# Optimization experiments

Measured on AMD Instinct MI355X. Metric: run time of the kernel, lower is better.

## Reference

```python
import jax, jax.numpy as jnp
import numpy as np

B, S, D, H, FF = 2, 2048, 1024, 16, 4096
HD = D // H          # head dim = 64
ROT = HD // 2        # rotary dim = dim/(num_heads*2) = 32 (partial rotation)
EPS = 1e-5


def setup_inputs() -> dict:
    key = jax.random.key(0)
    ks = jax.random.split(key, 16)
    std = 0.02
    return {
        "x": jax.random.normal(ks[0], (B, S, D), jnp.float32),
        "mask": jnp.ones((B, 1, 1, S), jnp.int32),
        "wq": jax.random.normal(ks[1], (D, D), jnp.float32) * std,
        "bq": jnp.zeros((D,), jnp.float32),
        "wk": jax.random.normal(ks[2], (D, D), jnp.float32) * std,
        "bk": jnp.zeros((D,), jnp.float32),
        "wv": jax.random.normal(ks[3], (D, D), jnp.float32) * std,
        "bv": jnp.zeros((D,), jnp.float32),
        "wo": jax.random.normal(ks[4], (D, D), jnp.float32) * std,
        "bo": jnp.zeros((D,), jnp.float32),
        "ln1_w": jnp.ones((D,), jnp.float32),
        "ln1_b": jnp.zeros((D,), jnp.float32),
        "ln2_w": jnp.ones((D,), jnp.float32),
        "ln2_b": jnp.zeros((D,), jnp.float32),
        "w1": jax.random.normal(ks[5], (D, FF), jnp.float32) * std,
        "b1": jnp.zeros((FF,), jnp.float32),
        "w2": jax.random.normal(ks[6], (FF, D), jnp.float32) * std,
        "b2": jnp.zeros((D,), jnp.float32),
    }


def _layernorm(x, w, b):
    mu = jnp.mean(x, axis=-1, keepdims=True)
    var = jnp.mean(jnp.square(x - mu), axis=-1, keepdims=True)
    return (x - mu) * jax.lax.rsqrt(var + EPS) * w + b


def _rope(t):
    # t: [B, H, S, HD]; rotate first ROT features, interleaved (GPT-J) pairing
    inv_freq = 1.0 / (10000.0 ** (jnp.arange(0, ROT, 2, dtype=jnp.float32) / ROT))
    ang = jnp.arange(S, dtype=jnp.float32)[:, None] * inv_freq      # [S, ROT//2]
    ang = jnp.repeat(ang, 2, axis=-1)                               # [S, ROT]
    cos, sin = jnp.cos(ang), jnp.sin(ang)
    t_rot, t_pass = t[..., :ROT], t[..., ROT:]
    pr = t_rot.reshape(*t_rot.shape[:-1], ROT // 2, 2)
    rot = jnp.stack([-pr[..., 1], pr[..., 0]], axis=-1).reshape(t_rot.shape)
    return jnp.concatenate([t_rot * cos + rot * sin, t_pass], axis=-1)


def reference(x, mask, wq, bq, wk, bk, wv, bv, wo, bo,
              ln1_w, ln1_b, ln2_w, ln2_b, w1, b1, w2, b2):
    res = x
    h = _layernorm(x, ln1_w, ln1_b)
    q = (h @ wq + bq).reshape(B, S, H, HD).transpose(0, 2, 1, 3)
    k = (h @ wk + bk).reshape(B, S, H, HD).transpose(0, 2, 1, 3)
    v = (h @ wv + bv).reshape(B, S, H, HD).transpose(0, 2, 1, 3)
    q, k = _rope(q), _rope(k)
    score = jnp.einsum('bhqd,bhkd->bhqk', q, k) * (1.0 / np.sqrt(HD))
    score = jnp.where(mask == 0, jnp.float32(-1e9), score)
    attn = jax.nn.softmax(score, axis=-1)
    out = jnp.einsum('bhqk,bhkd->bhqd', attn, v)
    out = out.transpose(0, 2, 1, 3).reshape(B, S, D) @ wo + bo
    x = res + out
    res = x
    h = _layernorm(x, ln2_w, ln2_b)
    h = jax.nn.gelu(h @ w1 + b1, approximate=False) @ w2 + b2
    return res + h
```

## Files before the change

### kernel.cpp

```cpp
#include <hip/hip_runtime.h>
#include <cstdint>
#include <cstddef>


typedef __bf16 bf16;
typedef __bf16 bf16x2 __attribute__((ext_vector_type(2)));
typedef __bf16 bf16x4v __attribute__((ext_vector_type(4)));
typedef __bf16 bf16x8 __attribute__((ext_vector_type(8)));
typedef float  f32x4  __attribute__((ext_vector_type(4)));

#define NB 2
#define NS 2048
#define ND 1024
#define NH 16
#define NHD 64
#define NFF 4096
#define NM (NB*NS)
#define QKSCALE 0.18033688011112042f

typedef uint32_t __attribute__((address_space(1))) gu32_t;
typedef uint32_t __attribute__((address_space(3))) lu32_t;
__device__ __forceinline__ void async_copy16(void* lds, const void* g) {
  __builtin_amdgcn_global_load_lds((gu32_t*)g, (lu32_t*)lds, 16, 0, 0);
}

__device__ __forceinline__ float gelu_f(float x) {
  return 0.5f * x * (1.0f + erff(x * 0.70710678118654752f));
}

__global__ __launch_bounds__(256) void prep_kernel(
    const float* __restrict__ wq, const float* __restrict__ wk,
    const float* __restrict__ wv, const float* __restrict__ wo,
    const float* __restrict__ w1, const float* __restrict__ w2,
    bf16* __restrict__ wqt, bf16* __restrict__ wkt, bf16* __restrict__ wvt,
    bf16* __restrict__ wot, bf16* __restrict__ w1t, bf16* __restrict__ w2t,
    const float* __restrict__ bq, const float* __restrict__ bk,
    const float* __restrict__ bv, float* __restrict__ bcat,
    const int* __restrict__ mask, float* __restrict__ m01f,
    bf16* __restrict__ m01b, float2* __restrict__ rtab,
    const float* __restrict__ x, const float* __restrict__ ln1w,
    const float* __restrict__ ln1b, bf16* __restrict__ h1) {
  int flat = blockIdx.x;
  int t = threadIdx.x;
  if (flat < 12288) {
    __shared__ float tile[32][33];
    const float* W; bf16* Wt; long bx, by; int K, N;
    if (flat < 4096) {
      int which = flat >> 10, r = flat & 1023;
      const float* Ws[4] = {wq, wk, wv, wo};
      bf16* Wts[4] = {wqt, wkt, wvt, wot};
      W = Ws[which]; Wt = Wts[which]; bx = r & 31; by = r >> 5; K = ND; N = ND;
    } else if (flat < 8192) {
      int r = flat - 4096;
      W = w1; Wt = w1t; bx = r & 127; by = r >> 7; K = ND; N = NFF;
    } else {
      int r = flat - 8192;
      W = w2; Wt = w2t; bx = r & 31; by = r >> 5; K = NFF; N = ND;
    }
    int tx = t & 31, ty = t >> 5;
#pragma unroll
    for (int r = 0; r < 4; ++r)
      tile[ty + r*8][tx] = W[(by*32 + ty + r*8) * (long)N + bx*32 + tx];
    __syncthreads();
#pragma unroll
    for (int r = 0; r < 4; ++r)
      Wt[(bx*32 + ty + r*8) * (long)K + by*32 + tx] = (bf16)tile[tx][ty + r*8];
  } else if (flat < 12444) {
    int blk = flat - 12288;
    if (blk < 12) {
      int i = blk * 256 + t;
      bcat[i] = (i < ND) ? bq[i] : ((i < 2*ND) ? bk[i - ND] : bv[i - 2*ND]);
    } else if (blk < 28) {
      int i = (blk - 12) * 256 + t;
      float v = mask[i] ? 1.0f : 0.0f;
      m01f[i] = v;
      m01b[i] = (bf16)v;
    } else {
      int idx = (blk - 28) * 256 + t;
      int s = idx >> 4, i = idx & 15;
      float ang = (float)s * exp2f(-(float)i * (13.287712379549449f / 16.0f));
      float sn, cs;
      sincosf(ang, &sn, &cs);
      rtab[idx] = make_float2(cs, sn);
    }
  } else {
    long row = flat - 12444;
    float4 v = ((const float4*)(x + row*ND))[t];
    float s  = v.x + v.y + v.z + v.w;
    float sq = v.x*v.x + v.y*v.y + v.z*v.z + v.w*v.w;
#pragma unroll
    for (int m = 1; m <= 32; m <<= 1) { s += __shfl_xor(s, m); sq += __shfl_xor(sq, m); }
    __shared__ float ss[4], ssq[4];
    if ((t & 63) == 0) { ss[t>>6] = s; ssq[t>>6] = sq; }
    __syncthreads();
    s  = ss[0] + ss[1] + ss[2] + ss[3];
    sq = ssq[0] + ssq[1] + ssq[2] + ssq[3];
    float mu = s * (1.0f/ND);
    float rs = rsqrtf(sq * (1.0f/ND) - mu*mu + 1e-5f);
    float4 wv4 = ((const float4*)ln1w)[t];
    float4 bv4 = ((const float4*)ln1b)[t];
    bf16x4v o;
    o[0] = (bf16)((v.x-mu)*rs*wv4.x + bv4.x);
    o[1] = (bf16)((v.y-mu)*rs*wv4.y + bv4.y);
    o[2] = (bf16)((v.z-mu)*rs*wv4.z + bv4.z);
    o[3] = (bf16)((v.w-mu)*rs*wv4.w + bv4.w);
    *(bf16x4v*)(h1 + row*ND + t*4) = o;
  }
}

__global__ __launch_bounds__(256) void vtrans_kernel(
    const bf16* __restrict__ v, bf16* __restrict__ vt) {
  __shared__ bf16 t[64][66];
  int st = blockIdx.x, bh = blockIdx.y;
  int b = bh >> 4, h = bh & 15;
  int c = threadIdx.x & 63, rg = threadIdx.x >> 6;
  const bf16* src = v + ((long)b*NS + st*64)*ND + h*64;
#pragma unroll
  for (int i = 0; i < 16; ++i) {
    int r = rg*16 + i;
    t[r][c] = src[(long)r*ND + c];
  }
  __syncthreads();
  bf16* dst = vt + (long)bh*64*NS + st*64;
#pragma unroll
  for (int i = 0; i < 16; ++i) {
    int d = rg*16 + i;
    dst[(long)d*NS + c] = t[c][d];
  }
}

__global__ __launch_bounds__(256) void ln_kernel(
    const float* __restrict__ x, const float* __restrict__ w,
    const float* __restrict__ b, bf16* __restrict__ out) {
  long row = blockIdx.x;
  int t = threadIdx.x;
  float4 v = ((const float4*)(x + row*ND))[t];
  float s  = v.x + v.y + v.z + v.w;
  float sq = v.x*v.x + v.y*v.y + v.z*v.z + v.w*v.w;
#pragma unroll
  for (int m = 1; m <= 32; m <<= 1) { s += __shfl_xor(s, m); sq += __shfl_xor(sq, m); }
  __shared__ float ss[4], ssq[4];
  if ((t & 63) == 0) { ss[t>>6] = s; ssq[t>>6] = sq; }
  __syncthreads();
  s  = ss[0] + ss[1] + ss[2] + ss[3];
  sq = ssq[0] + ssq[1] + ssq[2] + ssq[3];
  float mu = s * (1.0f/ND);
  float rs = rsqrtf(sq * (1.0f/ND) - mu*mu + 1e-5f);
  float4 wv = ((const float4*)w)[t];
  float4 bv = ((const float4*)b)[t];
  bf16x4v o;
  o[0] = (bf16)((v.x-mu)*rs*wv.x + bv.x);
  o[1] = (bf16)((v.y-mu)*rs*wv.y + bv.y);
  o[2] = (bf16)((v.z-mu)*rs*wv.z + bv.z);
  o[3] = (bf16)((v.w-mu)*rs*wv.w + bv.w);
  *(bf16x4v*)(out + row*ND + t*4) = o;
}

template<int EPI>
__global__ __launch_bounds__(512, 2) void gemm256_kernel(
    const bf16* __restrict__ A, const bf16* __restrict__ Bt,
    const float* __restrict__ bias, void* __restrict__ Cout,
    const float2* __restrict__ rtab, const float* __restrict__ m01f,
    int M, int N, int K) {
  __shared__ __align__(16) bf16 Alds[2][256*32];
  __shared__ __align__(16) bf16 Blds[2][256*32];
  const int tid = threadIdx.x, lane = tid & 63, w = tid >> 6;
  const int fr = lane & 15, kg = lane >> 4;
  const int wr = w >> 2, wc = w & 3;
  const int swb = (kg ^ ((fr >> 1) & 3)) << 4;

  const int gx = gridDim.x;
  int lin = blockIdx.y * gx + blockIdx.x;
  int nwg = gx * gridDim.y;
  int swz = (lin & 7) * (nwg >> 3) + (lin >> 3);
  const long am0 = (long)(swz / gx) * 256;
  const long bn0 = (long)(swz % gx) * 256;

  const f32x4 fzero = {0.f, 0.f, 0.f, 0.f};
  f32x4 acc[8][4];
#pragma unroll
  for (int m = 0; m < 8; ++m)
#pragma unroll
    for (int n = 0; n < 4; ++n) acc[m][n] = fzero;

  auto stage = [&](int kt, int bufi) {
#pragma unroll
    for (int i = 0; i < 2; ++i) {
      int s = i*512 + tid;
      int r = s >> 2, c = (s & 3) ^ ((s >> 3) & 3);
      async_copy16((char*)&Alds[bufi][0] + i*8192 + w*1024,
                   &A[(am0 + r)*K + kt + c*8]);
      async_copy16((char*)&Blds[bufi][0] + i*8192 + w*1024,
                   &Bt[(bn0 + r)*K + kt + c*8]);
    }
  };

  const int nk = K >> 5;
  stage(0, 0);
  asm volatile("s_waitcnt vmcnt(0)" ::: "memory");
  __builtin_amdgcn_s_barrier();
  __builtin_amdgcn_sched_barrier(0);

  for (int t = 0; t < nk; ++t) {
    const int cur = t & 1;
    if (t + 1 < nk) stage((t + 1) * 32, cur ^ 1);
    const char* Ab = (const char*)&Alds[cur][0];
    const char* Bb = (const char*)&Blds[cur][0];
    bf16x8 af[4], bfv[4];
#pragma unroll
    for (int n = 0; n < 4; ++n) bfv[n] = *(const bf16x8*)(Bb + (wc*64 + n*16 + fr)*64 + swb);
#pragma unroll
    for (int m = 0; m < 4; ++m) af[m]  = *(const bf16x8*)(Ab + (wr*128 + m*16 + fr)*64 + swb);
    asm volatile("s_waitcnt lgkmcnt(0)" ::: "memory");
    __builtin_amdgcn_sched_barrier(0);
    __builtin_amdgcn_s_setprio(1);
#pragma unroll
    for (int m = 0; m < 4; ++m)
#pragma unroll
      for (int n = 0; n < 4; ++n)
        acc[m][n] = __builtin_amdgcn_mfma_f32_16x16x32_bf16(af[m], bfv[n], acc[m][n], 0, 0, 0);
    __builtin_amdgcn_s_setprio(0);
#pragma unroll
    for (int m = 0; m < 4; ++m) af[m] = *(const bf16x8*)(Ab + (wr*128 + (m+4)*16 + fr)*64 + swb);
    asm volatile("s_waitcnt lgkmcnt(0)" ::: "memory");
    __builtin_amdgcn_sched_barrier(0);
    __builtin_amdgcn_s_setprio(1);
#pragma unroll
    for (int m = 0; m < 4; ++m)
#pragma unroll
      for (int n = 0; n < 4; ++n)
        acc[m+4][n] = __builtin_amdgcn_mfma_f32_16x16x32_bf16(af[m], bfv[n], acc[m+4][n], 0, 0, 0);
    __builtin_amdgcn_s_setprio(0);
    asm volatile("s_waitcnt vmcnt(0)" ::: "memory");
    __builtin_amdgcn_s_barrier();
    __builtin_amdgcn_sched_barrier(0);
  }

  const int rbase = kg * 4;
  const int region = (int)(bn0 >> 10);
#pragma unroll
  for (int m = 0; m < 8; ++m) {
#pragma unroll
    for (int n = 0; n < 4; ++n) {
      long col = bn0 + wc*64 + n*16 + fr;
      float bia = bias[col];
#pragma unroll
      for (int j = 0; j < 4; ++j) {
        long row = am0 + wr*128 + m*16 + rbase + j;
        float val = acc[m][n][j] + bia;
        if (EPI == 1) {
          ((bf16*)Cout)[row * N + col] = (bf16)gelu_f(val);
        } else {
          long cv = col & 1023;
          if (region <= 1) {
            float pval = __shfl_xor(val, 1);
            if (n < 2) {
              float2 cs = rtab[((row & (NS-1)) << 4) | ((n*16 + fr) >> 1)];
              val = (fr & 1) ? val*cs.x + pval*cs.y : val*cs.x - pval*cs.y;
            }
            if (region == 0) val *= QKSCALE;
          } else {
            val *= m01f[row];
          }
          ((bf16*)Cout)[(long)region * (NM*(long)ND) + row * ND + cv] = (bf16)val;
        }
      }
    }
  }
}

__global__ __launch_bounds__(512, 1) void gemm128x8_kernel(
    const bf16* __restrict__ A, const bf16* __restrict__ Bt,
    const float* __restrict__ bias, const float* __restrict__ res,
    float* __restrict__ Cout, int M, int N, int K) {
  __shared__ __align__(16) bf16 Alds[4][128*64];
  __shared__ __align__(16) bf16 Blds[4][128*64];
  const int tid = threadIdx.x, lane = tid & 63, w = tid >> 6;
  const int fr = lane & 15, kg = lane >> 4;
  const int wr = w >> 1, wc = w & 1;

  const int gx = gridDim.x;
  int lin = blockIdx.y * gx + blockIdx.x;
  int nwg = gx * gridDim.y;
  int swz = (lin & 7) * (nwg >> 3) + (lin >> 3);
  const long am0 = (long)(swz / gx) * 128;
  const long bn0 = (long)(swz % gx) * 128;

  const f32x4 fzero = {0.f, 0.f, 0.f, 0.f};
  f32x4 acc[2][4];
#pragma unroll
  for (int m = 0; m < 2; ++m)
#pragma unroll
    for (int n = 0; n < 4; ++n) acc[m][n] = fzero;

  auto stage = [&](int kt, int bufi) {
#pragma unroll
    for (int i = 0; i < 2; ++i) {
      int s = i*512 + tid;
      int r = s >> 3, c = (s & 7) ^ (r & 7);
      async_copy16((char*)&Alds[bufi][0] + i*8192 + w*1024,
                   &A[(am0 + r)*K + kt + c*8]);
      async_copy16((char*)&Blds[bufi][0] + i*8192 + w*1024,
                   &Bt[(bn0 + r)*K + kt + c*8]);
    }
  };

  const int nk = K >> 6;
  stage(0, 0);
  stage(64, 1);
  asm volatile("s_waitcnt vmcnt(4)" ::: "memory");
  __builtin_amdgcn_s_barrier();
  __builtin_amdgcn_sched_barrier(0);

  for (int t = 0; t < nk; ++t) {
    const int cur = t & 3;
    if (t + 2 < nk) stage((t + 2) * 64, (t + 2) & 3);
    const char* Ab = (const char*)&Alds[cur][0];
    const char* Bb = (const char*)&Blds[cur][0];
    bf16x8 af[2][2], bfv[2][4];
#pragma unroll
    for (int kk = 0; kk < 2; ++kk) {
#pragma unroll
      for (int m = 0; m < 2; ++m) {
        int r = wr*32 + m*16 + fr;
        af[kk][m] = *(const bf16x8*)(Ab + r*128 + (((kk*4 + kg) ^ (r & 7)) << 4));
      }
#pragma unroll
      for (int n = 0; n < 4; ++n) {
        int r = wc*64 + n*16 + fr;
        bfv[kk][n] = *(const bf16x8*)(Bb + r*128 + (((kk*4 + kg) ^ (r & 7)) << 4));
      }
    }
    asm volatile("s_waitcnt lgkmcnt(0)" ::: "memory");
    __builtin_amdgcn_sched_barrier(0);
    __builtin_amdgcn_s_setprio(1);
#pragma unroll
    for (int kk = 0; kk < 2; ++kk)
#pragma unroll
      for (int m = 0; m < 2; ++m)
#pragma unroll
        for (int n = 0; n < 4; ++n)
          acc[m][n] = __builtin_amdgcn_mfma_f32_16x16x32_bf16(af[kk][m], bfv[kk][n], acc[m][n], 0, 0, 0);
    __builtin_amdgcn_s_setprio(0);
    if (t + 2 < nk) { asm volatile("s_waitcnt vmcnt(4)" ::: "memory"); }
    else            { asm volatile("s_waitcnt vmcnt(0)" ::: "memory"); }
    __builtin_amdgcn_s_barrier();
    __builtin_amdgcn_sched_barrier(0);
  }

  const int rbase = kg * 4;
#pragma unroll
  for (int m = 0; m < 2; ++m) {
#pragma unroll
    for (int n = 0; n < 4; ++n) {
      long col = bn0 + wc*64 + n*16 + fr;
      float bia = bias[col];
#pragma unroll
      for (int j = 0; j < 4; ++j) {
        long row = am0 + wr*32 + m*16 + rbase + j;
        Cout[row * N + col] = acc[m][n][j] + bia + res[row * N + col];
      }
    }
  }
}

__global__ __launch_bounds__(512) void attn_kernel(
    const bf16* __restrict__ q, const bf16* __restrict__ k,
    const bf16* __restrict__ vt, const bf16* __restrict__ m01b,
    bf16* __restrict__ out) {
  int lin = blockIdx.y * 16 + blockIdx.x;
  int swz = (lin & 7) * 64 + (lin >> 3);
  const int qt = swz & 15;
  const int bh = swz >> 4;
  const int b = bh >> 4, h = bh & 15;
  const int tid = threadIdx.x, lane = tid & 63, w = tid >> 6;
  const int fr = lane & 15, kg = lane >> 4;
  const int k8 = kg * 8;
  const int frl = fr & 3, frh = fr >> 2;

  __shared__ __align__(16) bf16 Klds[3][64*64];
  __shared__ __align__(16) bf16 Vlds[3][64*64];
  __shared__ __align__(16) bf16 Mlds[NS];

  const long qrow = (long)qt*128 + w*16 + fr;
  const bf16* qbase = q + ((long)b*NS + qrow)*ND + h*NHD;
  bf16x8 qf[2];
  qf[0] = *(const bf16x8*)(qbase + k8);
  qf[1] = *(const bf16x8*)(qbase + 32 + k8);

  const bf16* kbase = k + (long)b*NS*ND + h*NHD;
  const bf16* vtb = vt + (long)bh*64*NS;
  const bf16* mbase = m01b + (long)b*NS;

  if (w < 4) async_copy16((char*)Mlds + w*1024, mbase + tid*8);

  const int srow = tid >> 3, sc = tid & 7;
  const int csK = (sc ^ (srow & 7) ^ (((srow >> 3) & 1) << 2));
  const int csV = (sc ^ (srow & 7));
  auto stageK = [&](int kt, int bufi) {
    async_copy16((char*)&Klds[bufi][0] + w*1024,
                 kbase + ((long)kt*64 + srow)*ND + csK*8);
  };
  auto stageV = [&](int kt, int bufi) {
    async_copy16((char*)&Vlds[bufi][0] + w*1024,
                 vtb + (long)srow*NS + kt*64 + csV*8);
  };

  const f32x4 fzero = {0.f, 0.f, 0.f, 0.f};
  f32x4 oacc[4], oaccL = fzero;
#pragma unroll
  for (int n = 0; n < 4; ++n) oacc[n] = fzero;

  stageK(0, 0); stageV(0, 0);
  stageK(1, 1); stageV(1, 1);
  asm volatile("s_waitcnt vmcnt(2)" ::: "memory");
  __builtin_amdgcn_s_barrier();
  __builtin_amdgcn_sched_barrier(0);

  const int NT = NS / 64;
  int bcur = 0, bpre = 1;
  for (int kt = 0; kt < NT; ++kt) {
    if (kt + 2 < NT) {
      bpre = (bpre == 2) ? 0 : bpre + 1;
      stageK(kt + 2, bpre);
      stageV(kt + 2, bpre);
    }
    const char* Kb = (const char*)&Klds[bcur][0];
    const char* Vb = (const char*)&Vlds[bcur][0];

    bf16x8 vbm0 = *(const bf16x8*)&Mlds[kt*64 + k8];
    bf16x8 vbm1 = *(const bf16x8*)&Mlds[kt*64 + 32 + k8];

    f32x4 sacc[4];
#pragma unroll
    for (int n = 0; n < 4; ++n) sacc[n] = fzero;
#pragma unroll
    for (int n = 0; n < 4; ++n) {
      int r = (frh << 3) + ((n & 1) << 2) + frl + ((n >> 1) << 5);
      int swzr = (r & 7) ^ (((r >> 3) & 1) << 2);
#pragma unroll
      for (int kk = 0; kk < 2; ++kk) {
        bf16x8 kf = *(const bf16x8*)(Kb + r*128 + ((((kk << 2) | kg) ^ swzr) << 4));
        sacc[n] = __builtin_amdgcn_mfma_f32_16x16x32_bf16(kf, qf[kk], sacc[n], 0, 0, 0);
      }
    }

    float p[4][4];
#pragma unroll
    for (int n = 0; n < 4; ++n) {
      p[n][0] = exp2f(sacc[n][0]);
      p[n][1] = exp2f(sacc[n][1]);
      p[n][2] = exp2f(sacc[n][2]);
      p[n][3] = exp2f(sacc[n][3]);
    }

    bf16x8 paf[2];
#pragma unroll
    for (int n = 0; n < 4; ++n) {
#pragma unroll
      for (int j = 0; j < 4; ++j)
        paf[n >> 1][((n & 1) << 2) + j] = (bf16)p[n][j];
    }

    oaccL = __builtin_amdgcn_mfma_f32_16x16x32_bf16(paf[0], vbm0, oaccL, 0, 0, 0);
    oaccL = __builtin_amdgcn_mfma_f32_16x16x32_bf16(paf[1], vbm1, oaccL, 0, 0, 0);

#pragma unroll
    for (int kk = 0; kk < 2; ++kk) {
#pragma unroll
      for (int n2 = 0; n2 < 4; ++n2) {
        int r = n2*16 + fr;
        bf16x8 vb8 = *(const bf16x8*)(Vb + r*128 + ((((kk << 2) | kg) ^ (r & 7)) << 4));
        oacc[n2] = __builtin_amdgcn_mfma_f32_16x16x32_bf16(paf[kk], vb8, oacc[n2], 0, 0, 0);
      }
    }

    if (kt + 2 < NT)      { asm volatile("s_waitcnt vmcnt(2)" ::: "memory"); }
    else if (kt + 1 < NT) { asm volatile("s_waitcnt vmcnt(0)" ::: "memory"); }
    __builtin_amdgcn_s_barrier();
    __builtin_amdgcn_sched_barrier(0);
    bcur = (bcur == 2) ? 0 : bcur + 1;
  }

#pragma unroll
  for (int j = 0; j < 4; ++j) {
    float inv = 1.0f / oaccL[j];
    long orow = (long)qt*128 + w*16 + kg*4 + j;
    bf16* ob = out + ((long)b*NS + orow)*ND + h*NHD;
#pragma unroll
    for (int n2 = 0; n2 < 4; ++n2) ob[n2*16 + fr] = (bf16)(oacc[n2][j] * inv);
  }
}

extern "C" void kernel_launch(void* const* d_in, const int* in_sizes, int n_in,
                              void* d_out, int out_size, void* d_ws, size_t ws_size,
                              hipStream_t stream) {
  const float* x    = (const float*)d_in[0];
  const int*   mask = (const int*)d_in[1];
  const float* wq   = (const float*)d_in[2];
  const float* bq   = (const float*)d_in[3];
  const float* wk   = (const float*)d_in[4];
  const float* bk   = (const float*)d_in[5];
  const float* wv   = (const float*)d_in[6];
  const float* bv   = (const float*)d_in[7];
  const float* wo   = (const float*)d_in[8];
  const float* bo   = (const float*)d_in[9];
  const float* ln1w = (const float*)d_in[10];
  const float* ln1b = (const float*)d_in[11];
  const float* ln2w = (const float*)d_in[12];
  const float* ln2b = (const float*)d_in[13];
  const float* w1   = (const float*)d_in[14];
  const float* b1   = (const float*)d_in[15];
  const float* w2   = (const float*)d_in[16];
  const float* b2   = (const float*)d_in[17];
  float* out = (float*)d_out;

  char* ws = (char*)d_ws;
  const size_t MB = 1024ull * 1024ull;
  bf16* wqt = (bf16*)(ws + 0*MB);
  bf16* wkt = (bf16*)(ws + 2*MB);
  bf16* wvt = (bf16*)(ws + 4*MB);
  bf16* wot = (bf16*)(ws + 6*MB);
  bf16* w1t = (bf16*)(ws + 8*MB);
  bf16* w2t = (bf16*)(ws + 16*MB);
  bf16* h1   = (bf16*)(ws + 24*MB);
  bf16* qb   = (bf16*)(ws + 32*MB);
  bf16* kb   = (bf16*)(ws + 40*MB);
  bf16* vb   = (bf16*)(ws + 48*MB);
  bf16* vtb  = h1;
  bf16* attnb = (bf16*)(ws + 72*MB);
  bf16* f1   = (bf16*)(ws + 24*MB);
  float* y1  = (float*)(ws + 56*MB);
  bf16* h2   = (bf16*)(ws + 72*MB);
  float* bcat = (float*)(ws + 80*MB);
  float* m01f = (float*)(ws + 80*MB + 16*1024);
  bf16*  m01b = (bf16*) (ws + 80*MB + 32*1024);
  float2* rtab = (float2*)(ws + 80*MB + 48*1024);
  (void)in_sizes; (void)n_in; (void)out_size; (void)ws_size;

  prep_kernel<<<16540, 256, 0, stream>>>(wq, wk, wv, wo, w1, w2,
                                         wqt, wkt, wvt, wot, w1t, w2t,
                                         bq, bk, bv, bcat, mask, m01f, m01b,
                                         rtab, x, ln1w, ln1b, h1);

  gemm256_kernel<3><<<dim3(12, 16), 512, 0, stream>>>(h1, wqt, bcat, qb,
                                                      rtab, m01f, NM, 3*ND, ND);
  vtrans_kernel<<<dim3(32, 32), 256, 0, stream>>>(vb, vtb);

  attn_kernel<<<dim3(16, 32), 512, 0, stream>>>(qb, kb, vtb, m01b, attnb);

  gemm128x8_kernel<<<dim3(8, 32), 512, 0, stream>>>(attnb, wot, bo, x, y1,
                                                    NM, ND, ND);
  ln_kernel<<<NM, 256, 0, stream>>>(y1, ln2w, ln2b, h2);
  gemm256_kernel<1><<<dim3(16, 16), 512, 0, stream>>>(h2, w1t, b1, f1,
                                                      nullptr, nullptr, NM, NFF, ND);
  gemm128x8_kernel<<<dim3(8, 32), 512, 0, stream>>>(f1, w2t, b2, y1, out,
                                                    NM, ND, NFF);
}
```

Measured before the change: 289.5 us.

## Split-K the FFN down-projection GEMM with fp32 partials and reduction kernel

```diff
diff --git a/kernel.cpp b/kernel.cpp
--- a/kernel.cpp
+++ b/kernel.cpp
@@ -156,18 +156,42 @@
   *(bf16x4v*)(out + row*ND + t*4) = o;
 }
 
+__global__ __launch_bounds__(256) void ffn2red_kernel(
+    const float* __restrict__ P, const float* __restrict__ y1,
+    const float* __restrict__ b2, float* __restrict__ out) {
+  const long n4 = (long)NM * ND / 4;
+  const float4* p = (const float4*)P;
+  const float4* y = (const float4*)y1;
+  const float4* bb = (const float4*)b2;
+  float4* o = (float4*)out;
+  for (long i = (long)blockIdx.x*256 + threadIdx.x; i < n4;
+       i += (long)gridDim.x*256) {
+    float4 a0 = p[i], a1 = p[i + n4], a2 = p[i + 2*n4], a3 = p[i + 3*n4];
+    float4 yv = y[i];
+    float4 bv = bb[i & 255];
+    float4 r;
+    r.x = (a0.x + a1.x) + (a2.x + a3.x) + yv.x + bv.x;
+    r.y = (a0.y + a1.y) + (a2.y + a3.y) + yv.y + bv.y;
+    r.z = (a0.z + a1.z) + (a2.z + a3.z) + yv.z + bv.z;
+    r.w = (a0.w + a1.w) + (a2.w + a3.w) + yv.w + bv.w;
+    o[i] = r;
+  }
+}
+
 template<int EPI>
 __global__ __launch_bounds__(512, 2) void gemm256_kernel(
     const bf16* __restrict__ A, const bf16* __restrict__ Bt,
     const float* __restrict__ bias, void* __restrict__ Cout,
     const float2* __restrict__ rtab, const float* __restrict__ m01f,
-    int M, int N, int K) {
+    int M, int N, int K, int lda, int ldbt) {
   __shared__ __align__(16) bf16 Alds[2][256*32];
   __shared__ __align__(16) bf16 Blds[2][256*32];
   const int tid = threadIdx.x, lane = tid & 63, w = tid >> 6;
   const int fr = lane & 15, kg = lane >> 4;
   const int wr = w >> 2, wc = w & 3;
   const int swb = (kg ^ ((fr >> 1) & 3)) << 4;
+  const int kz = (EPI == 2) ? blockIdx.z : 0;
+  const long kofs = (long)kz * K;
 
   const int gx = gridDim.x;
   int lin = blockIdx.y * gx + blockIdx.x;
@@ -189,9 +213,9 @@
       int s = i*512 + tid;
       int r = s >> 2, c = (s & 3) ^ ((s >> 3) & 3);
       async_copy16((char*)&Alds[bufi][0] + i*8192 + w*1024,
-                   &A[(am0 + r)*K + kt + c*8]);
+                   &A[(am0 + r)*(long)lda + kofs + kt + c*8]);
       async_copy16((char*)&Blds[bufi][0] + i*8192 + w*1024,
-                   &Bt[(bn0 + r)*K + kt + c*8]);
+                   &Bt[(bn0 + r)*(long)ldbt + kofs + kt + c*8]);
     }
   };
 
@@ -243,13 +267,15 @@
 #pragma unroll
     for (int n = 0; n < 4; ++n) {
       long col = bn0 + wc*64 + n*16 + fr;
-      float bia = bias[col];
+      float bia = (EPI == 2) ? 0.0f : bias[col];
 #pragma unroll
       for (int j = 0; j < 4; ++j) {
         long row = am0 + wr*128 + m*16 + rbase + j;
         float val = acc[m][n][j] + bia;
         if (EPI == 1) {
           ((bf16*)Cout)[row * N + col] = (bf16)gelu_f(val);
+        } else if (EPI == 2) {
+          ((float*)Cout)[((long)kz * NM + row) * N + col] = val;
         } else {
           long cv = col & 1023;
           if (region <= 1) {
@@ -536,7 +562,9 @@
   float* m01f = (float*)(ws + 80*MB + 16*1024);
   bf16*  m01b = (bf16*) (ws + 80*MB + 32*1024);
   float2* rtab = (float2*)(ws + 80*MB + 48*1024);
-  (void)in_sizes; (void)n_in; (void)out_size; (void)ws_size;
+  float* pK   = (float*)(ws + 84*MB);
+  const bool use_splitk = (ws_size >= 148ull*MB);
+  (void)in_sizes; (void)n_in; (void)out_size;
 
   prep_kernel<<<16540, 256, 0, stream>>>(wq, wk, wv, wo, w1, w2,
                                          wqt, wkt, wvt, wot, w1t, w2t,
@@ -544,7 +572,8 @@
                                          rtab, x, ln1w, ln1b, h1);
 
   gemm256_kernel<3><<<dim3(12, 16), 512, 0, stream>>>(h1, wqt, bcat, qb,
-                                                      rtab, m01f, NM, 3*ND, ND);
+                                                      rtab, m01f, NM, 3*ND, ND,
+                                                      ND, ND);
   vtrans_kernel<<<dim3(32, 32), 256, 0, stream>>>(vb, vtb);
 
   attn_kernel<<<dim3(16, 32), 512, 0, stream>>>(qb, kb, vtb, m01b, attnb);
@@ -553,7 +582,15 @@
                                                     NM, ND, ND);
   ln_kernel<<<NM, 256, 0, stream>>>(y1, ln2w, ln2b, h2);
   gemm256_kernel<1><<<dim3(16, 16), 512, 0, stream>>>(h2, w1t, b1, f1,
-                                                      nullptr, nullptr, NM, NFF, ND);
-  gemm128x8_kernel<<<dim3(8, 32), 512, 0, stream>>>(f1, w2t, b2, y1, out,
-                                                    NM, ND, NFF);
-}
+                                                      nullptr, nullptr,
+                                                      NM, NFF, ND, ND, ND);
+  if (use_splitk) {
+    gemm256_kernel<2><<<dim3(4, 16, 4), 512, 0, stream>>>(f1, w2t, nullptr, pK,
+                                                          nullptr, nullptr,
+                                                          NM, ND, ND, NFF, NFF);
+    ffn2red_kernel<<<2048, 256, 0, stream>>>(pK, y1, b2, out);
+  } else {
+    gemm128x8_kernel<<<dim3(8, 32), 512, 0, stream>>>(f1, w2t, b2, y1, out,
+                                                      NM, ND, NFF);
+  }
+}
```

After: 292.0 us. Within noise of the previous version (+0.9%).
